# Performance work log

Hardware: AMD Instinct MI355X
Metric: run time of the kernel (lower is better)

Reference implementation:

```python
import jax, jax.numpy as jnp
import numpy as np

FMAP = 32
HEADS = 8
DK = 32
DV = 64
N = FMAP * FMAP  # 1024 tokens
SCALE = DK ** -0.5


def conv1x1(x, W):
    # x: (b,c,h,w), W: (o,c) -> (b,o,h,w)
    return jnp.einsum('bchw,oc->bohw', x, W)


def bn(x, g, b):
    # inference-mode BatchNorm2d folded to per-channel affine
    return x * g[None, :, None, None] + b[None, :, None, None]


def pos_indices():
    r = jnp.arange(FMAP)
    ii, jj = jnp.meshgrid(r, r, indexing='ij')
    pos = jnp.stack([ii.reshape(-1), jj.reshape(-1)], axis=-1)  # (N,2)
    rel = jnp.abs(pos[:, None, :] - pos[None, :, :])            # (N,N,2)
    return rel[..., 0] * FMAP + rel[..., 1]                     # (N,N) int


def setup_inputs() -> dict:
    key = jax.random.key(0)
    ks = jax.random.split(key, 8)
    b, dim = 4, 256
    inner_k, inner_v = HEADS * DK, HEADS * DV
    s = lambda fan: 1.0 / np.sqrt(fan)
    return {
        'x': jax.random.normal(ks[0], (b, dim, FMAP, FMAP), jnp.float32),
        'Wq': jax.random.normal(ks[1], (inner_k, dim), jnp.float32) * s(dim),
        'gq': jnp.ones((inner_k,), jnp.float32), 'bq': jnp.zeros((inner_k,), jnp.float32),
        'Wk': jax.random.normal(ks[2], (inner_k, dim), jnp.float32) * s(dim),
        'gk': jnp.ones((inner_k,), jnp.float32), 'bk': jnp.zeros((inner_k,), jnp.float32),
        'Wv': jax.random.normal(ks[3], (inner_v, dim), jnp.float32) * s(dim),
        'gv': jnp.ones((inner_v,), jnp.float32), 'bv': jnp.zeros((inner_v,), jnp.float32),
        'Wmk': jax.random.normal(ks[4], (HEADS * N, inner_k), jnp.float32) * s(inner_k),
        'gmk': jnp.ones((HEADS * N,), jnp.float32), 'bmk': jnp.zeros((HEADS * N,), jnp.float32),
        'pos_emb': jax.random.normal(ks[5], (N, HEADS), jnp.float32),
        'Wo': jax.random.normal(ks[6], (dim, 2 * inner_v), jnp.float32) * s(2 * inner_v),
        'bo': jnp.zeros((dim,), jnp.float32),
        'go': jnp.ones((dim,), jnp.float32), 'bo2': jnp.zeros((dim,), jnp.float32),
    }


def reference(x, Wq, gq, bq, Wk, gk, bk, Wv, gv, bv, Wmk, gmk, bmk, pos_emb, Wo, bo, go, bo2):
    b = x.shape[0]
    idx = pos_indices()  # (N,N) static

    q1 = bn(conv1x1(x, Wq), gq, bq)                       # (b, h*dk, F, F)
    kk = bn(conv1x1(x, Wk), gk, bk)
    vv = bn(conv1x1(x, Wv), gv, bv)

    # 'b (h d) x y -> b h (x y) d'
    q = q1.reshape(b, HEADS, DK, N).transpose(0, 1, 3, 2)  # (b,h,n,dk)
    k = kk.reshape(b, HEADS, DK, N).transpose(0, 1, 3, 2)
    v = vv.reshape(b, HEADS, DV, N).transpose(0, 1, 3, 2)  # (b,h,n,dv)

    # branch 1: learned conv position logits + relative pos bias
    dots1 = bn(conv1x1(q1, Wmk), gmk, bmk)                 # (b, h*N, F, F)
    dots1 = dots1.reshape(b, HEADS, N, N).transpose(0, 1, 3, 2)  # (b,h,i,j)
    bias = pos_emb[idx]                                    # (N,N,h) gather
    dots1 = dots1 + jnp.transpose(bias, (2, 0, 1))[None] / SCALE
    attn1 = jax.nn.softmax(dots1, axis=-1)

    # branch 2: standard scaled dot-product attention
    dots2 = jnp.einsum('bhid,bhjd->bhij', q, k) * SCALE
    attn2 = jax.nn.softmax(dots2, axis=-1)

    out1 = jnp.einsum('bhij,bhjd->bhid', attn1, v)         # (b,h,n,dv)
    out2 = jnp.einsum('bhij,bhjd->bhid', attn2, v)
    # 'b h (x y) d -> b (h d) x y'
    out1 = out1.transpose(0, 1, 3, 2).reshape(b, HEADS * DV, FMAP, FMAP)
    out2 = out2.transpose(0, 1, 3, 2).reshape(b, HEADS * DV, FMAP, FMAP)

    out = jnp.concatenate([out1, out2], axis=1)            # (b, 2*h*dv, F, F)
    out = jax.nn.gelu(out, approximate=False)
    out = conv1x1(out, Wo) + bo[None, :, None, None]
    return bn(out, go, bo2)
```

## Files before the change

kernel.cpp:

```cpp
#include <hip/hip_runtime.h>

#define NHEADS 8
#define DKK    32
#define DVV    64
#define NTOK   1024
#define DIM    256

typedef float  f32x4 __attribute__((ext_vector_type(4)));
typedef short  s16x4 __attribute__((ext_vector_type(4)));
typedef short  s16x8 __attribute__((ext_vector_type(8)));

__device__ __forceinline__ unsigned short f2bf(float f) {
    unsigned u = __builtin_bit_cast(unsigned, f);
    u += 0x7FFFu + ((u >> 16) & 1u);
    return (unsigned short)(u >> 16);
}

__global__ __launch_bounds__(256) void conv_x(
    const float* __restrict__ x, short* __restrict__ xbt)
{
    __shared__ short tl[64 * 72];
    const int n0 = blockIdx.x * 64, c0 = blockIdx.y * 64, b = blockIdx.z;
    const int tid = threadIdx.x;
    #pragma unroll
    for (int s = 0; s < 16; ++s) {
        int id = tid + s * 256;
        int cc = id >> 6, nn = id & 63;
        tl[nn * 72 + cc] = (short)f2bf(x[(size_t)b * 262144 + (size_t)(c0 + cc) * 1024 + n0 + nn]);
    }
    __syncthreads();
    #pragma unroll
    for (int s = 0; s < 2; ++s) {
        int id = tid + s * 256;
        int nn = id >> 3, c8 = id & 7;
        *(s16x8*)(xbt + ((size_t)b * 1024 + n0 + nn) * 256 + c0 + c8 * 8) =
            *(const s16x8*)&tl[nn * 72 + c8 * 8];
    }
}

__global__ __launch_bounds__(256) void conv_wqkv(
    const float* __restrict__ Wq, const float* __restrict__ gq,
    const float* __restrict__ Wk, const float* __restrict__ gk,
    const float* __restrict__ Wv, const float* __restrict__ gv,
    short* __restrict__ wqkvb)
{
    const int sub = threadIdx.x >> 5;
    const int row = blockIdx.x * 8 + sub;
    const int c0  = (threadIdx.x & 31) * 8;
    float g; const float* src;
    if (row < 256)      { g = gq[row];       src = Wq + (size_t)row * DIM; }
    else if (row < 512) { g = gk[row - 256]; src = Wk + (size_t)(row - 256) * DIM; }
    else                { g = gv[row - 512]; src = Wv + (size_t)(row - 512) * DIM; }
    float4 x0 = *(const float4*)(src + c0);
    float4 x1 = *(const float4*)(src + c0 + 4);
    s16x8 o;
    o[0] = (short)f2bf(g * x0.x); o[1] = (short)f2bf(g * x0.y);
    o[2] = (short)f2bf(g * x0.z); o[3] = (short)f2bf(g * x0.w);
    o[4] = (short)f2bf(g * x1.x); o[5] = (short)f2bf(g * x1.y);
    o[6] = (short)f2bf(g * x1.z); o[7] = (short)f2bf(g * x1.w);
    *(s16x8*)(wqkvb + (size_t)row * DIM + c0) = o;
}

__global__ __launch_bounds__(256) void wmk_convert(
    const float* __restrict__ Wmk, const float* __restrict__ gmk,
    short* __restrict__ out)
{
    const int sub = threadIdx.x >> 5;
    const int ch  = blockIdx.x * 8 + sub;
    const int c0  = (threadIdx.x & 31) * 8;
    const float g = gmk[ch];
    const float* src = Wmk + (size_t)ch * DIM + c0;
    float4 x0 = *(const float4*)(src);
    float4 x1 = *(const float4*)(src + 4);
    s16x8 o;
    o[0] = (short)f2bf(g * x0.x); o[1] = (short)f2bf(g * x0.y);
    o[2] = (short)f2bf(g * x0.z); o[3] = (short)f2bf(g * x0.w);
    o[4] = (short)f2bf(g * x1.x); o[5] = (short)f2bf(g * x1.y);
    o[6] = (short)f2bf(g * x1.z); o[7] = (short)f2bf(g * x1.w);
    *(s16x8*)(out + (size_t)ch * DIM + c0) = o;
}

__global__ __launch_bounds__(256) void conv_wo(
    const float* __restrict__ Wo, short* __restrict__ wob)
{
    const int sub = threadIdx.x >> 5;
    const int row = blockIdx.x * 8 + sub;
    const int l   = threadIdx.x & 31;
    #pragma unroll
    for (int u = 0; u < 4; ++u) {
        int c = l * 8 + u * 256;
        const float* src = Wo + (size_t)row * 1024 + c;
        float4 x0 = *(const float4*)(src);
        float4 x1 = *(const float4*)(src + 4);
        s16x8 o;
        o[0] = (short)f2bf(x0.x); o[1] = (short)f2bf(x0.y);
        o[2] = (short)f2bf(x0.z); o[3] = (short)f2bf(x0.w);
        o[4] = (short)f2bf(x1.x); o[5] = (short)f2bf(x1.y);
        o[6] = (short)f2bf(x1.z); o[7] = (short)f2bf(x1.w);
        *(s16x8*)(wob + (size_t)row * 1024 + c) = o;
    }
}

__global__ __launch_bounds__(256) void qkv_mfma(
    const short* __restrict__ wqkvb, const short* __restrict__ xbt,
    const float* __restrict__ bq, const float* __restrict__ bk,
    const float* __restrict__ bv,
    short* __restrict__ qk_t, short* __restrict__ vvb)
{
    __shared__ __align__(16) short tlds[64 * 136];

    const int t0 = blockIdx.x * 64;
    const int c0 = blockIdx.y * 128;
    const int tid  = threadIdx.x;
    const int w    = tid >> 6, lane = tid & 63;
    const int l15  = lane & 15, lhi = lane >> 4;
    const int wr = w >> 1, wc = w & 1;
    const int cob = c0 + wr * 64;
    const int tob = t0 + wc * 32;

    f32x4 acc[4][2];
    #pragma unroll
    for (int mf = 0; mf < 4; ++mf)
        #pragma unroll
        for (int nf = 0; nf < 2; ++nf) acc[mf][nf] = (f32x4){0.f, 0.f, 0.f, 0.f};

    #pragma unroll
    for (int ks = 0; ks < 8; ++ks) {
        s16x8 af[4], bf[2];
        #pragma unroll
        for (int mf = 0; mf < 4; ++mf)
            af[mf] = *(const s16x8*)(wqkvb + (size_t)(cob + mf * 16 + l15) * DIM + ks * 32 + lhi * 8);
        #pragma unroll
        for (int nf = 0; nf < 2; ++nf)
            bf[nf] = *(const s16x8*)(xbt + (size_t)(tob + nf * 16 + l15) * DIM + ks * 32 + lhi * 8);
        #pragma unroll
        for (int mf = 0; mf < 4; ++mf)
            #pragma unroll
            for (int nf = 0; nf < 2; ++nf)
                acc[mf][nf] = __builtin_amdgcn_mfma_f32_16x16x32_bf16(af[mf], bf[nf], acc[mf][nf], 0, 0, 0);
    }

    float bias[4][4];
    #pragma unroll
    for (int mf = 0; mf < 4; ++mf)
        #pragma unroll
        for (int q = 0; q < 4; ++q) {
            int ch = cob + mf * 16 + lhi * 4 + q;
            bias[mf][q] = (ch < 256) ? bq[ch] : (ch < 512) ? bk[ch - 256] : bv[ch - 512];
        }

    if (c0 < 512) {
        #pragma unroll
        for (int mf = 0; mf < 4; ++mf)
            #pragma unroll
            for (int nf = 0; nf < 2; ++nf) {
                s16x4 pk;
                #pragma unroll
                for (int q = 0; q < 4; ++q)
                    pk[q] = (short)f2bf(acc[mf][nf][q] + bias[mf][q]);
                int tokl = wc * 32 + nf * 16 + l15;
                int chl  = wr * 64 + mf * 16 + lhi * 4;
                *(s16x4*)&tlds[tokl * 136 + chl] = pk;
            }
        __syncthreads();
        #pragma unroll
        for (int s = 0; s < 4; ++s) {
            int id = tid + s * 256;
            int tok = id >> 4, c8 = id & 15;
            *(s16x8*)(qk_t + (size_t)(t0 + tok) * 512 + c0 + c8 * 8) =
                *(const s16x8*)&tlds[tok * 136 + c8 * 8];
        }
    } else {
        #pragma unroll
        for (int mf = 0; mf < 4; ++mf)
            #pragma unroll
            for (int nf = 0; nf < 2; ++nf) {
                int gt = tob + nf * 16 + l15;
                #pragma unroll
                for (int q = 0; q < 4; ++q) {
                    int vch = cob + mf * 16 + lhi * 4 + q - 512;
                    vvb[(size_t)vch * 4096 + gt] = (short)f2bf(acc[mf][nf][q] + bias[mf][q]);
                }
            }
    }
}

__global__ __launch_bounds__(512, 2) void attn_kernel(
    const short* __restrict__ qk_t, const short* __restrict__ vvb,
    const short* __restrict__ wmkb, const float* __restrict__ bmk,
    const float* __restrict__ pos_emb, short* __restrict__ gbuf)
{
    __shared__ __align__(16) short wmks[64 * 264];
    __shared__ __align__(16) short ps[8 * 16 * 72];
    __shared__ float pe_s[1024];
    __shared__ float bmk_s[1024];

    const int it = blockIdx.x, h = blockIdx.y, b = blockIdx.z;
    const int i0  = it * 128;
    const int tid = threadIdx.x;
    const int w    = tid >> 6;
    const int lane = tid & 63;
    const int l15  = lane & 15;
    const int lhi  = lane >> 4;

    for (int p = tid; p < 1024; p += 512) {
        pe_s[p]  = pos_emb[p * NHEADS + h] * 5.656854249492380f;
        bmk_s[p] = bmk[h * NTOK + p];
    }

    const short* q1row = qk_t + ((size_t)b * NTOK + i0 + w * 16 + l15) * 512;
    s16x8 a1[8];
    #pragma unroll
    for (int ks = 0; ks < 8; ++ks)
        a1[ks] = *(const s16x8*)(q1row + ks * 32 + lhi * 8);
    s16x8 a2 = *(const s16x8*)(q1row + h * DKK + lhi * 8);

    int ixq[4], iyq[4];
    #pragma unroll
    for (int q = 0; q < 4; ++q) {
        int i = i0 + w * 16 + lhi * 4 + q;
        ixq[q] = i >> 5; iyq[q] = i & 31;
    }

    f32x4 o1[4], o2[4];
    #pragma unroll
    for (int df = 0; df < 4; ++df)
        #pragma unroll
        for (int q = 0; q < 4; ++q) { o1[df][q] = 0.0f; o2[df][q] = 0.0f; }
    float m1[4], l1[4], m2[4], l2[4];
    #pragma unroll
    for (int q = 0; q < 4; ++q) { m1[q] = -INFINITY; l1[q] = 0.f; m2[q] = -INFINITY; l2[q] = 0.f; }

    const short* kbase = qk_t + (size_t)b * NTOK * 512 + 256 + h * DKK;
    const short* vbase = vvb + (size_t)(h * DVV) * 4096 + b * NTOK;
    const short* wbase = wmkb + (size_t)h * NTOK * DIM;
    short* psw = ps + w * 16 * 72;
    const float SCALE = 0.17677669529663687f;

    __syncthreads();

    for (int jc = 0; jc < 16; ++jc) {
        const int j0 = jc * 64;
        __syncthreads();

        #pragma unroll
        for (int s = 0; s < 4; ++s) {
            int m = tid + s * 512;
            int row = m >> 5, ch = m & 31;
            s16x8 v = *(const s16x8*)(wbase + (size_t)(j0 + row) * DIM + ch * 8);
            *(s16x8*)(&wmks[row * 264 + ch * 8]) = v;
        }
        __syncthreads();

        s16x8 b2f[4], vf[2][4];
        #pragma unroll
        for (int df = 0; df < 4; ++df) {
            b2f[df] = *(const s16x8*)(kbase + (size_t)(j0 + df * 16 + l15) * 512 + lhi * 8);
            #pragma unroll
            for (int ks = 0; ks < 2; ++ks)
                vf[ks][df] = *(const s16x8*)(vbase + (size_t)(df * 16 + l15) * 4096 + j0 + ks * 32 + lhi * 8);
        }

        f32x4 s1[4];
        #pragma unroll
        for (int df = 0; df < 4; ++df) {
            f32x4 acc = {0.f, 0.f, 0.f, 0.f};
            #pragma unroll
            for (int ks = 0; ks < 8; ++ks) {
                s16x8 bfr = *(const s16x8*)(&wmks[(df * 16 + l15) * 264 + ks * 32 + lhi * 8]);
                acc = __builtin_amdgcn_mfma_f32_16x16x32_bf16(a1[ks], bfr, acc, 0, 0, 0);
            }
            s1[df] = acc;
        }
        #pragma unroll
        for (int df = 0; df < 4; ++df) {
            int j  = j0 + df * 16 + l15;
            float bv = bmk_s[j];
            int jx = j >> 5, jy = j & 31;
            #pragma unroll
            for (int q = 0; q < 4; ++q) {
                int dx = ixq[q] - jx; dx = dx < 0 ? -dx : dx;
                int dy = iyq[q] - jy; dy = dy < 0 ? -dy : dy;
                s1[df][q] += bv + pe_s[dx * 32 + dy];
            }
        }
        #pragma unroll
        for (int q = 0; q < 4; ++q) {
            float mx = fmaxf(fmaxf(s1[0][q], s1[1][q]), fmaxf(s1[2][q], s1[3][q]));
            #pragma unroll
            for (int off = 1; off < 16; off <<= 1) mx = fmaxf(mx, __shfl_xor(mx, off, 64));
            float mnew = fmaxf(m1[q], mx);
            float sc = __expf(m1[q] - mnew);
            float rs = 0.f;
            #pragma unroll
            for (int df = 0; df < 4; ++df) {
                float p = __expf(s1[df][q] - mnew);
                rs += p;
                psw[(lhi * 4 + q) * 72 + df * 16 + l15] = (short)f2bf(p);
                o1[df][q] *= sc;
            }
            #pragma unroll
            for (int off = 1; off < 16; off <<= 1) rs += __shfl_xor(rs, off, 64);
            l1[q] = l1[q] * sc + rs;
            m1[q] = mnew;
        }
        {
            s16x8 ap0 = *(const s16x8*)(&psw[l15 * 72 +  0 + lhi * 8]);
            s16x8 ap1 = *(const s16x8*)(&psw[l15 * 72 + 32 + lhi * 8]);
            #pragma unroll
            for (int df = 0; df < 4; ++df) {
                o1[df] = __builtin_amdgcn_mfma_f32_16x16x32_bf16(ap0, vf[0][df], o1[df], 0, 0, 0);
                o1[df] = __builtin_amdgcn_mfma_f32_16x16x32_bf16(ap1, vf[1][df], o1[df], 0, 0, 0);
            }
        }

        f32x4 s2[4];
        #pragma unroll
        for (int df = 0; df < 4; ++df) {
            f32x4 z = {0.f, 0.f, 0.f, 0.f};
            z = __builtin_amdgcn_mfma_f32_16x16x32_bf16(a2, b2f[df], z, 0, 0, 0);
            #pragma unroll
            for (int q = 0; q < 4; ++q) s2[df][q] = z[q] * SCALE;
        }
        #pragma unroll
        for (int q = 0; q < 4; ++q) {
            float mx = fmaxf(fmaxf(s2[0][q], s2[1][q]), fmaxf(s2[2][q], s2[3][q]));
            #pragma unroll
            for (int off = 1; off < 16; off <<= 1) mx = fmaxf(mx, __shfl_xor(mx, off, 64));
            float mnew = fmaxf(m2[q], mx);
            float sc = __expf(m2[q] - mnew);
            float rs = 0.f;
            #pragma unroll
            for (int df = 0; df < 4; ++df) {
                float p = __expf(s2[df][q] - mnew);
                rs += p;
                psw[(lhi * 4 + q) * 72 + df * 16 + l15] = (short)f2bf(p);
                o2[df][q] *= sc;
            }
            #pragma unroll
            for (int off = 1; off < 16; off <<= 1) rs += __shfl_xor(rs, off, 64);
            l2[q] = l2[q] * sc + rs;
            m2[q] = mnew;
        }
        {
            s16x8 ap0 = *(const s16x8*)(&psw[l15 * 72 +  0 + lhi * 8]);
            s16x8 ap1 = *(const s16x8*)(&psw[l15 * 72 + 32 + lhi * 8]);
            #pragma unroll
            for (int df = 0; df < 4; ++df) {
                o2[df] = __builtin_amdgcn_mfma_f32_16x16x32_bf16(ap0, vf[0][df], o2[df], 0, 0, 0);
                o2[df] = __builtin_amdgcn_mfma_f32_16x16x32_bf16(ap1, vf[1][df], o2[df], 0, 0, 0);
            }
        }
    }

    short* osw = wmks;
    #pragma unroll
    for (int pass = 0; pass < 2; ++pass) {
        __syncthreads();
        const int chbase = pass == 0 ? h * DVV : 512 + h * DVV;
        #pragma unroll
        for (int df = 0; df < 4; ++df)
            #pragma unroll
            for (int q = 0; q < 4; ++q) {
                float v = (pass == 0 ? o1[df][q] / l1[q] : o2[df][q] / l2[q]);
                v = 0.5f * v * (1.0f + erff(v * 0.70710678118654752f));
                osw[(w * 16 + lhi * 4 + q) * 72 + df * 16 + l15] = (short)f2bf(v);
            }
        __syncthreads();
        #pragma unroll
        for (int s = 0; s < 2; ++s) {
            int id = tid + s * 512;
            int tok = id >> 3, c8 = id & 7;
            *(s16x8*)(gbuf + ((size_t)b * NTOK + i0 + tok) * 1024 + chbase + c8 * 8) =
                *(const s16x8*)&osw[tok * 72 + c8 * 8];
        }
    }
}

__global__ __launch_bounds__(256) void out_mfma(
    const short* __restrict__ wob, const short* __restrict__ gbuf,
    const float* __restrict__ bo, const float* __restrict__ go,
    const float* __restrict__ bo2, float* __restrict__ out)
{
    const int t0 = blockIdx.x * 64;
    const int c0 = blockIdx.y * 64;
    const int tid  = threadIdx.x;
    const int w    = tid >> 6, lane = tid & 63;
    const int l15  = lane & 15, lhi = lane >> 4;
    const int wr = w >> 1, wc = w & 1;
    const int cob = c0 + wr * 32;
    const int tob = t0 + wc * 32;

    f32x4 acc[2][2];
    #pragma unroll
    for (int mf = 0; mf < 2; ++mf)
        #pragma unroll
        for (int nf = 0; nf < 2; ++nf) acc[mf][nf] = (f32x4){0.f, 0.f, 0.f, 0.f};

    #pragma unroll 4
    for (int ks = 0; ks < 32; ++ks) {
        s16x8 af[2], bf[2];
        #pragma unroll
        for (int mf = 0; mf < 2; ++mf)
            af[mf] = *(const s16x8*)(wob + (size_t)(cob + mf * 16 + l15) * 1024 + ks * 32 + lhi * 8);
        #pragma unroll
        for (int nf = 0; nf < 2; ++nf)
            bf[nf] = *(const s16x8*)(gbuf + (size_t)(tob + nf * 16 + l15) * 1024 + ks * 32 + lhi * 8);
        #pragma unroll
        for (int mf = 0; mf < 2; ++mf)
            #pragma unroll
            for (int nf = 0; nf < 2; ++nf)
                acc[mf][nf] = __builtin_amdgcn_mfma_f32_16x16x32_bf16(af[mf], bf[nf], acc[mf][nf], 0, 0, 0);
    }

    #pragma unroll
    for (int mf = 0; mf < 2; ++mf) {
        #pragma unroll
        for (int q = 0; q < 4; ++q) {
            int co = cob + mf * 16 + lhi * 4 + q;
            float bov = bo[co], gov = go[co], bo2v = bo2[co];
            #pragma unroll
            for (int nf = 0; nf < 2; ++nf) {
                int gt = tob + nf * 16 + l15;
                int bb = gt >> 10, n = gt & 1023;
                out[(size_t)bb * 262144 + (size_t)co * 1024 + n] =
                    fmaf(acc[mf][nf][q] + bov, gov, bo2v);
            }
        }
    }
}

extern "C" void kernel_launch(void* const* d_in, const int* in_sizes, int n_in,
                              void* d_out, int out_size, void* d_ws, size_t ws_size,
                              hipStream_t stream)
{
    const float* x    = (const float*)d_in[0];
    const float* Wq   = (const float*)d_in[1];
    const float* gq   = (const float*)d_in[2];
    const float* bq   = (const float*)d_in[3];
    const float* Wk   = (const float*)d_in[4];
    const float* gk   = (const float*)d_in[5];
    const float* bk   = (const float*)d_in[6];
    const float* Wv   = (const float*)d_in[7];
    const float* gv   = (const float*)d_in[8];
    const float* bv   = (const float*)d_in[9];
    const float* Wmk  = (const float*)d_in[10];
    const float* gmk  = (const float*)d_in[11];
    const float* bmk  = (const float*)d_in[12];
    const float* pe   = (const float*)d_in[13];
    const float* Wo   = (const float*)d_in[14];
    const float* bo   = (const float*)d_in[15];
    const float* go   = (const float*)d_in[16];
    const float* bo2  = (const float*)d_in[17];
    float* out = (float*)d_out;

    char* base = (char*)d_ws;
    short* xbt   = (short*)(base);
    short* wqkvb = (short*)(base + (2u  << 20));
    short* wmkb  = (short*)(base + (3u  << 20));
    short* wob   = (short*)(base + (7u  << 20));
    short* qk_t  = (short*)(base + (8u  << 20));
    short* vvb   = (short*)(base + (12u << 20));
    short* gbuf  = (short*)(base + (16u << 20));

    conv_x<<<dim3(16, 4, 4), 256, 0, stream>>>(x, xbt);
    conv_wqkv<<<dim3(128), 256, 0, stream>>>(Wq, gq, Wk, gk, Wv, gv, wqkvb);
    wmk_convert<<<dim3(1024), 256, 0, stream>>>(Wmk, gmk, wmkb);
    conv_wo<<<dim3(32), 256, 0, stream>>>(Wo, wob);
    qkv_mfma<<<dim3(64, 8), 256, 0, stream>>>(wqkvb, xbt, bq, bk, bv, qk_t, vvb);
    attn_kernel<<<dim3(8, NHEADS, 4), 512, 0, stream>>>(qk_t, vvb, wmkb, bmk, pe, gbuf);
    out_mfma<<<dim3(64, 4), 256, 0, stream>>>(wob, gbuf, bo, go, bo2, out);
}
```

Baseline: 143.1 us.

## Restructure attention with transposed MFMA, register softmax, lazy rescale, and smaller tiles

Rewrites the attention kernel so scores are computed transposed (keys as rows), which keeps the softmax reduction mostly in registers and moves probabilities into the PV MFMA by cross-lane shuffles instead of an LDS round trip. It also prefetches the next Wmk tile into registers during compute, skips the running-max rescale unless the max grows by more than 8, folds the QK scale into the K weights, and uses packed bf16 conversion. The QKV, attention and output GEMMs get smaller tiles and more blocks so more blocks are in flight. Risks include extra register pressure, shuffle overhead, and the lazy-rescale precision tradeoff.

```diff
diff --git a/kernel.cpp b/kernel.cpp
--- a/kernel.cpp
+++ b/kernel.cpp
@@ -9,11 +9,24 @@
 typedef float  f32x4 __attribute__((ext_vector_type(4)));
 typedef short  s16x4 __attribute__((ext_vector_type(4)));
 typedef short  s16x8 __attribute__((ext_vector_type(8)));
+typedef int    i32x4 __attribute__((ext_vector_type(4)));
+
+#define SCALE_QK 0.17677669529663687f
 
 __device__ __forceinline__ unsigned short f2bf(float f) {
     unsigned u = __builtin_bit_cast(unsigned, f);
     u += 0x7FFFu + ((u >> 16) & 1u);
     return (unsigned short)(u >> 16);
+}
+
+__device__ __forceinline__ unsigned cvt_pk_bf16(float lo, float hi) {
+    unsigned r;
+    asm("v_cvt_pk_bf16_f32 %0, %1, %2" : "=v"(r) : "v"(lo), "v"(hi));
+    return r;
+}
+
+__device__ __forceinline__ float gelu(float v) {
+    return 0.5f * v * (1.0f + erff(v * 0.70710678118654752f));
 }
 
 __global__ __launch_bounds__(256) void conv_x(
@@ -48,9 +61,9 @@
     const int row = blockIdx.x * 8 + sub;
     const int c0  = (threadIdx.x & 31) * 8;
     float g; const float* src;
-    if (row < 256)      { g = gq[row];       src = Wq + (size_t)row * DIM; }
-    else if (row < 512) { g = gk[row - 256]; src = Wk + (size_t)(row - 256) * DIM; }
-    else                { g = gv[row - 512]; src = Wv + (size_t)(row - 512) * DIM; }
+    if (row < 256)      { g = gq[row];                  src = Wq + (size_t)row * DIM; }
+    else if (row < 512) { g = gk[row - 256] * SCALE_QK; src = Wk + (size_t)(row - 256) * DIM; }
+    else                { g = gv[row - 512];            src = Wv + (size_t)(row - 512) * DIM; }
     float4 x0 = *(const float4*)(src + c0);
     float4 x1 = *(const float4*)(src + c0 + 4);
     s16x8 o;
@@ -107,64 +120,62 @@
     const float* __restrict__ bv,
     short* __restrict__ qk_t, short* __restrict__ vvb)
 {
-    __shared__ __align__(16) short tlds[64 * 136];
-
-    const int t0 = blockIdx.x * 64;
+    __shared__ __align__(16) short tlds[32 * 136];
+
+    const int t0 = blockIdx.x * 32;
     const int c0 = blockIdx.y * 128;
     const int tid  = threadIdx.x;
     const int w    = tid >> 6, lane = tid & 63;
     const int l15  = lane & 15, lhi = lane >> 4;
-    const int wr = w >> 1, wc = w & 1;
-    const int cob = c0 + wr * 64;
-    const int tob = t0 + wc * 32;
-
-    f32x4 acc[4][2];
-    #pragma unroll
-    for (int mf = 0; mf < 4; ++mf)
+    const int cob = c0 + w * 32;
+
+    f32x4 acc[2][2];
+    #pragma unroll
+    for (int mf = 0; mf < 2; ++mf)
         #pragma unroll
         for (int nf = 0; nf < 2; ++nf) acc[mf][nf] = (f32x4){0.f, 0.f, 0.f, 0.f};
 
     #pragma unroll
     for (int ks = 0; ks < 8; ++ks) {
-        s16x8 af[4], bf[2];
-        #pragma unroll
-        for (int mf = 0; mf < 4; ++mf)
+        s16x8 af[2], bf[2];
+        #pragma unroll
+        for (int mf = 0; mf < 2; ++mf)
             af[mf] = *(const s16x8*)(wqkvb + (size_t)(cob + mf * 16 + l15) * DIM + ks * 32 + lhi * 8);
         #pragma unroll
         for (int nf = 0; nf < 2; ++nf)
-            bf[nf] = *(const s16x8*)(xbt + (size_t)(tob + nf * 16 + l15) * DIM + ks * 32 + lhi * 8);
-        #pragma unroll
-        for (int mf = 0; mf < 4; ++mf)
+            bf[nf] = *(const s16x8*)(xbt + (size_t)(t0 + nf * 16 + l15) * DIM + ks * 32 + lhi * 8);
+        #pragma unroll
+        for (int mf = 0; mf < 2; ++mf)
             #pragma unroll
             for (int nf = 0; nf < 2; ++nf)
                 acc[mf][nf] = __builtin_amdgcn_mfma_f32_16x16x32_bf16(af[mf], bf[nf], acc[mf][nf], 0, 0, 0);
     }
 
-    float bias[4][4];
-    #pragma unroll
-    for (int mf = 0; mf < 4; ++mf)
+    float bias[2][4];
+    #pragma unroll
+    for (int mf = 0; mf < 2; ++mf)
         #pragma unroll
         for (int q = 0; q < 4; ++q) {
             int ch = cob + mf * 16 + lhi * 4 + q;
-            bias[mf][q] = (ch < 256) ? bq[ch] : (ch < 512) ? bk[ch - 256] : bv[ch - 512];
+            bias[mf][q] = (ch < 256) ? bq[ch]
+                        : (ch < 512) ? bk[ch - 256] * SCALE_QK
+                                     : bv[ch - 512];
         }
 
     if (c0 < 512) {
         #pragma unroll
-        for (int mf = 0; mf < 4; ++mf)
+        for (int mf = 0; mf < 2; ++mf)
             #pragma unroll
             for (int nf = 0; nf < 2; ++nf) {
                 s16x4 pk;
                 #pragma unroll
                 for (int q = 0; q < 4; ++q)
                     pk[q] = (short)f2bf(acc[mf][nf][q] + bias[mf][q]);
-                int tokl = wc * 32 + nf * 16 + l15;
-                int chl  = wr * 64 + mf * 16 + lhi * 4;
-                *(s16x4*)&tlds[tokl * 136 + chl] = pk;
+                *(s16x4*)&tlds[(nf * 16 + l15) * 136 + w * 32 + mf * 16 + lhi * 4] = pk;
             }
         __syncthreads();
         #pragma unroll
-        for (int s = 0; s < 4; ++s) {
+        for (int s = 0; s < 2; ++s) {
             int id = tid + s * 256;
             int tok = id >> 4, c8 = id & 15;
             *(s16x8*)(qk_t + (size_t)(t0 + tok) * 512 + c0 + c8 * 8) =
@@ -172,10 +183,10 @@
         }
     } else {
         #pragma unroll
-        for (int mf = 0; mf < 4; ++mf)
+        for (int mf = 0; mf < 2; ++mf)
             #pragma unroll
             for (int nf = 0; nf < 2; ++nf) {
-                int gt = tob + nf * 16 + l15;
+                int gt = t0 + nf * 16 + l15;
                 #pragma unroll
                 for (int q = 0; q < 4; ++q) {
                     int vch = cob + mf * 16 + lhi * 4 + q - 512;
@@ -185,171 +196,206 @@
     }
 }
 
-__global__ __launch_bounds__(512, 2) void attn_kernel(
+__global__ __launch_bounds__(256, 2) void attn_kernel(
     const short* __restrict__ qk_t, const short* __restrict__ vvb,
     const short* __restrict__ wmkb, const float* __restrict__ bmk,
     const float* __restrict__ pos_emb, short* __restrict__ gbuf)
 {
     __shared__ __align__(16) short wmks[64 * 264];
-    __shared__ __align__(16) short ps[8 * 16 * 72];
     __shared__ float pe_s[1024];
     __shared__ float bmk_s[1024];
 
-    const int it = blockIdx.x, h = blockIdx.y, b = blockIdx.z;
-    const int i0  = it * 128;
+    const int flat = blockIdx.x;
+    const int h  = flat & 7;
+    const int it = (flat >> 3) & 15;
+    const int b  = flat >> 7;
+    const int i0 = it * 64;
     const int tid = threadIdx.x;
-    const int w    = tid >> 6;
-    const int lane = tid & 63;
-    const int l15  = lane & 15;
-    const int lhi  = lane >> 4;
-
-    for (int p = tid; p < 1024; p += 512) {
+    const int w = tid >> 6, lane = tid & 63;
+    const int l15 = lane & 15, lhi = lane >> 4;
+
+    for (int p = tid; p < 1024; p += 256) {
         pe_s[p]  = pos_emb[p * NHEADS + h] * 5.656854249492380f;
         bmk_s[p] = bmk[h * NTOK + p];
     }
 
-    const short* q1row = qk_t + ((size_t)b * NTOK + i0 + w * 16 + l15) * 512;
+    const int irow = i0 + w * 16 + l15;
+    const short* q1row = qk_t + ((size_t)b * NTOK + irow) * 512;
     s16x8 a1[8];
     #pragma unroll
     for (int ks = 0; ks < 8; ++ks)
         a1[ks] = *(const s16x8*)(q1row + ks * 32 + lhi * 8);
     s16x8 a2 = *(const s16x8*)(q1row + h * DKK + lhi * 8);
 
-    int ixq[4], iyq[4];
+    const int ix = irow >> 5, iy = irow & 31;
+    int dyv0[4], dyv1[4];
     #pragma unroll
     for (int q = 0; q < 4; ++q) {
-        int i = i0 + w * 16 + lhi * 4 + q;
-        ixq[q] = i >> 5; iyq[q] = i & 31;
+        int j0y = lhi * 4 + q, j1y = 16 + lhi * 4 + q;
+        dyv0[q] = (iy >= j0y) ? iy - j0y : j0y - iy;
+        dyv1[q] = (iy >= j1y) ? iy - j1y : j1y - iy;
     }
 
     f32x4 o1[4], o2[4];
     #pragma unroll
-    for (int df = 0; df < 4; ++df)
-        #pragma unroll
-        for (int q = 0; q < 4; ++q) { o1[df][q] = 0.0f; o2[df][q] = 0.0f; }
-    float m1[4], l1[4], m2[4], l2[4];
-    #pragma unroll
-    for (int q = 0; q < 4; ++q) { m1[q] = -INFINITY; l1[q] = 0.f; m2[q] = -INFINITY; l2[q] = 0.f; }
+    for (int df = 0; df < 4; ++df) { o1[df] = (f32x4){0.f,0.f,0.f,0.f}; o2[df] = (f32x4){0.f,0.f,0.f,0.f}; }
+    float m1 = -INFINITY, l1 = 0.0f, m2 = -INFINITY, l2 = 0.0f;
 
     const short* kbase = qk_t + (size_t)b * NTOK * 512 + 256 + h * DKK;
     const short* vbase = vvb + (size_t)(h * DVV) * 4096 + b * NTOK;
     const short* wbase = wmkb + (size_t)h * NTOK * DIM;
-    short* psw = ps + w * 16 * 72;
-    const float SCALE = 0.17677669529663687f;
-
-    __syncthreads();
+
+    const int srow = tid >> 2;
+    const int scol = (tid & 3) * 64;
+    s16x8 stg[8];
+    #pragma unroll
+    for (int u = 0; u < 8; ++u)
+        stg[u] = *(const s16x8*)(wbase + (size_t)srow * DIM + scol + u * 8);
 
     for (int jc = 0; jc < 16; ++jc) {
         const int j0 = jc * 64;
         __syncthreads();
-
-        #pragma unroll
-        for (int s = 0; s < 4; ++s) {
-            int m = tid + s * 512;
-            int row = m >> 5, ch = m & 31;
-            s16x8 v = *(const s16x8*)(wbase + (size_t)(j0 + row) * DIM + ch * 8);
-            *(s16x8*)(&wmks[row * 264 + ch * 8]) = v;
-        }
+        #pragma unroll
+        for (int u = 0; u < 8; ++u)
+            *(s16x8*)&wmks[srow * 264 + scol + u * 8] = stg[u];
         __syncthreads();
-
-        s16x8 b2f[4], vf[2][4];
-        #pragma unroll
-        for (int df = 0; df < 4; ++df) {
-            b2f[df] = *(const s16x8*)(kbase + (size_t)(j0 + df * 16 + l15) * 512 + lhi * 8);
-            #pragma unroll
-            for (int ks = 0; ks < 2; ++ks)
-                vf[ks][df] = *(const s16x8*)(vbase + (size_t)(df * 16 + l15) * 4096 + j0 + ks * 32 + lhi * 8);
-        }
-
-        f32x4 s1[4];
+        if (jc < 15) {
+            #pragma unroll
+            for (int u = 0; u < 8; ++u)
+                stg[u] = *(const s16x8*)(wbase + (size_t)(j0 + 64 + srow) * DIM + scol + u * 8);
+        }
+
+        s16x8 b2a[4];
+        #pragma unroll
+        for (int df = 0; df < 4; ++df)
+            b2a[df] = *(const s16x8*)(kbase + (size_t)(j0 + df * 16 + l15) * 512 + lhi * 8);
+
+        f32x4 s1T[4];
         #pragma unroll
         for (int df = 0; df < 4; ++df) {
             f32x4 acc = {0.f, 0.f, 0.f, 0.f};
             #pragma unroll
             for (int ks = 0; ks < 8; ++ks) {
-                s16x8 bfr = *(const s16x8*)(&wmks[(df * 16 + l15) * 264 + ks * 32 + lhi * 8]);
-                acc = __builtin_amdgcn_mfma_f32_16x16x32_bf16(a1[ks], bfr, acc, 0, 0, 0);
-            }
-            s1[df] = acc;
-        }
-        #pragma unroll
-        for (int df = 0; df < 4; ++df) {
-            int j  = j0 + df * 16 + l15;
-            float bv = bmk_s[j];
-            int jx = j >> 5, jy = j & 31;
-            #pragma unroll
-            for (int q = 0; q < 4; ++q) {
-                int dx = ixq[q] - jx; dx = dx < 0 ? -dx : dx;
-                int dy = iyq[q] - jy; dy = dy < 0 ? -dy : dy;
-                s1[df][q] += bv + pe_s[dx * 32 + dy];
-            }
-        }
-        #pragma unroll
-        for (int q = 0; q < 4; ++q) {
-            float mx = fmaxf(fmaxf(s1[0][q], s1[1][q]), fmaxf(s1[2][q], s1[3][q]));
-            #pragma unroll
-            for (int off = 1; off < 16; off <<= 1) mx = fmaxf(mx, __shfl_xor(mx, off, 64));
-            float mnew = fmaxf(m1[q], mx);
-            float sc = __expf(m1[q] - mnew);
-            float rs = 0.f;
-            #pragma unroll
-            for (int df = 0; df < 4; ++df) {
-                float p = __expf(s1[df][q] - mnew);
-                rs += p;
-                psw[(lhi * 4 + q) * 72 + df * 16 + l15] = (short)f2bf(p);
-                o1[df][q] *= sc;
-            }
-            #pragma unroll
-            for (int off = 1; off < 16; off <<= 1) rs += __shfl_xor(rs, off, 64);
-            l1[q] = l1[q] * sc + rs;
-            m1[q] = mnew;
-        }
-        {
-            s16x8 ap0 = *(const s16x8*)(&psw[l15 * 72 +  0 + lhi * 8]);
-            s16x8 ap1 = *(const s16x8*)(&psw[l15 * 72 + 32 + lhi * 8]);
-            #pragma unroll
-            for (int df = 0; df < 4; ++df) {
-                o1[df] = __builtin_amdgcn_mfma_f32_16x16x32_bf16(ap0, vf[0][df], o1[df], 0, 0, 0);
-                o1[df] = __builtin_amdgcn_mfma_f32_16x16x32_bf16(ap1, vf[1][df], o1[df], 0, 0, 0);
-            }
-        }
-
-        f32x4 s2[4];
+                s16x8 afr = *(const s16x8*)&wmks[(df * 16 + l15) * 264 + ks * 32 + lhi * 8];
+                acc = __builtin_amdgcn_mfma_f32_16x16x32_bf16(afr, a1[ks], acc, 0, 0, 0);
+            }
+            s1T[df] = acc;
+        }
+        f32x4 s2T[4];
         #pragma unroll
         for (int df = 0; df < 4; ++df) {
             f32x4 z = {0.f, 0.f, 0.f, 0.f};
-            z = __builtin_amdgcn_mfma_f32_16x16x32_bf16(a2, b2f[df], z, 0, 0, 0);
-            #pragma unroll
-            for (int q = 0; q < 4; ++q) s2[df][q] = z[q] * SCALE;
-        }
-        #pragma unroll
-        for (int q = 0; q < 4; ++q) {
-            float mx = fmaxf(fmaxf(s2[0][q], s2[1][q]), fmaxf(s2[2][q], s2[3][q]));
-            #pragma unroll
-            for (int off = 1; off < 16; off <<= 1) mx = fmaxf(mx, __shfl_xor(mx, off, 64));
-            float mnew = fmaxf(m2[q], mx);
-            float sc = __expf(m2[q] - mnew);
+            s2T[df] = __builtin_amdgcn_mfma_f32_16x16x32_bf16(b2a[df], a2, z, 0, 0, 0);
+        }
+
+        {
+            const int jx0 = j0 >> 5;
+            int d0 = ix - jx0;     d0 = d0 < 0 ? -d0 : d0;
+            int d1 = ix - jx0 - 1; d1 = d1 < 0 ? -d1 : d1;
+            const float* per0 = pe_s + d0 * 32;
+            const float* per1 = pe_s + d1 * 32;
+            #pragma unroll
+            for (int df = 0; df < 4; ++df) {
+                f32x4 bm4 = *(const f32x4*)&bmk_s[j0 + df * 16 + lhi * 4];
+                #pragma unroll
+                for (int q = 0; q < 4; ++q) {
+                    int dy = (df & 1) ? dyv1[q] : dyv0[q];
+                    float pv = (df < 2) ? per0[dy] : per1[dy];
+                    s1T[df][q] += bm4[q] + pv;
+                }
+            }
+        }
+
+        unsigned pk1[4][2];
+        {
+            float mx = s1T[0][0];
+            #pragma unroll
+            for (int df = 0; df < 4; ++df)
+                #pragma unroll
+                for (int q = 0; q < 4; ++q) mx = fmaxf(mx, s1T[df][q]);
+            mx = fmaxf(mx, __shfl_xor(mx, 16));
+            mx = fmaxf(mx, __shfl_xor(mx, 32));
+            float tm = fmaxf(m1, mx);
+            if (!__all(tm - m1 <= 8.0f)) {
+                float sc = __expf(m1 - tm);
+                l1 *= sc;
+                #pragma unroll
+                for (int df = 0; df < 4; ++df) o1[df] *= sc;
+                m1 = tm;
+            }
             float rs = 0.f;
             #pragma unroll
             for (int df = 0; df < 4; ++df) {
-                float p = __expf(s2[df][q] - mnew);
-                rs += p;
-                psw[(lhi * 4 + q) * 72 + df * 16 + l15] = (short)f2bf(p);
-                o2[df][q] *= sc;
-            }
-            #pragma unroll
-            for (int off = 1; off < 16; off <<= 1) rs += __shfl_xor(rs, off, 64);
-            l2[q] = l2[q] * sc + rs;
-            m2[q] = mnew;
-        }
+                float p0 = __expf(s1T[df][0] - m1), p1 = __expf(s1T[df][1] - m1);
+                float p2 = __expf(s1T[df][2] - m1), p3 = __expf(s1T[df][3] - m1);
+                rs += (p0 + p1) + (p2 + p3);
+                pk1[df][0] = cvt_pk_bf16(p0, p1);
+                pk1[df][1] = cvt_pk_bf16(p2, p3);
+            }
+            rs += __shfl_xor(rs, 16);
+            rs += __shfl_xor(rs, 32);
+            l1 += rs;
+        }
+        unsigned pk2[4][2];
         {
-            s16x8 ap0 = *(const s16x8*)(&psw[l15 * 72 +  0 + lhi * 8]);
-            s16x8 ap1 = *(const s16x8*)(&psw[l15 * 72 + 32 + lhi * 8]);
+            float mx = s2T[0][0];
+            #pragma unroll
+            for (int df = 0; df < 4; ++df)
+                #pragma unroll
+                for (int q = 0; q < 4; ++q) mx = fmaxf(mx, s2T[df][q]);
+            mx = fmaxf(mx, __shfl_xor(mx, 16));
+            mx = fmaxf(mx, __shfl_xor(mx, 32));
+            float tm = fmaxf(m2, mx);
+            if (!__all(tm - m2 <= 8.0f)) {
+                float sc = __expf(m2 - tm);
+                l2 *= sc;
+                #pragma unroll
+                for (int df = 0; df < 4; ++df) o2[df] *= sc;
+                m2 = tm;
+            }
+            float rs = 0.f;
             #pragma unroll
             for (int df = 0; df < 4; ++df) {
-                o2[df] = __builtin_amdgcn_mfma_f32_16x16x32_bf16(ap0, vf[0][df], o2[df], 0, 0, 0);
-                o2[df] = __builtin_amdgcn_mfma_f32_16x16x32_bf16(ap1, vf[1][df], o2[df], 0, 0, 0);
-            }
+                float p0 = __expf(s2T[df][0] - m2), p1 = __expf(s2T[df][1] - m2);
+                float p2 = __expf(s2T[df][2] - m2), p3 = __expf(s2T[df][3] - m2);
+                rs += (p0 + p1) + (p2 + p3);
+                pk2[df][0] = cvt_pk_bf16(p0, p1);
+                pk2[df][1] = cvt_pk_bf16(p2, p3);
+            }
+            rs += __shfl_xor(rs, 16);
+            rs += __shfl_xor(rs, 32);
+            l2 += rs;
+        }
+
+        const int srcA = l15 + ((lane & 16) << 1);
+        const bool hi = (lane & 32) != 0;
+        #pragma unroll
+        for (int kt = 0; kt < 2; ++kt) {
+            s16x8 vf[4];
+            #pragma unroll
+            for (int df = 0; df < 4; ++df)
+                vf[df] = *(const s16x8*)(vbase + (size_t)(df * 16 + l15) * 4096 + j0 + kt * 32 + lhi * 8);
+
+            int x0 = __shfl((int)pk1[2*kt][0], srcA),      x1 = __shfl((int)pk1[2*kt+1][0], srcA);
+            int y0 = __shfl((int)pk1[2*kt][1], srcA),      y1 = __shfl((int)pk1[2*kt+1][1], srcA);
+            int z0 = __shfl((int)pk1[2*kt][0], srcA + 16), z1 = __shfl((int)pk1[2*kt+1][0], srcA + 16);
+            int u0 = __shfl((int)pk1[2*kt][1], srcA + 16), u1 = __shfl((int)pk1[2*kt+1][1], srcA + 16);
+            i32x4 bd1 = { hi ? x1 : x0, hi ? y1 : y0, hi ? z1 : z0, hi ? u1 : u0 };
+            s16x8 pb1 = __builtin_bit_cast(s16x8, bd1);
+
+            x0 = __shfl((int)pk2[2*kt][0], srcA);      x1 = __shfl((int)pk2[2*kt+1][0], srcA);
+            y0 = __shfl((int)pk2[2*kt][1], srcA);      y1 = __shfl((int)pk2[2*kt+1][1], srcA);
+            z0 = __shfl((int)pk2[2*kt][0], srcA + 16); z1 = __shfl((int)pk2[2*kt+1][0], srcA + 16);
+            u0 = __shfl((int)pk2[2*kt][1], srcA + 16); u1 = __shfl((int)pk2[2*kt+1][1], srcA + 16);
+            i32x4 bd2 = { hi ? x1 : x0, hi ? y1 : y0, hi ? z1 : z0, hi ? u1 : u0 };
+            s16x8 pb2 = __builtin_bit_cast(s16x8, bd2);
+
+            #pragma unroll
+            for (int df = 0; df < 4; ++df)
+                o1[df] = __builtin_amdgcn_mfma_f32_16x16x32_bf16(vf[df], pb1, o1[df], 0, 0, 0);
+            #pragma unroll
+            for (int df = 0; df < 4; ++df)
+                o2[df] = __builtin_amdgcn_mfma_f32_16x16x32_bf16(vf[df], pb2, o2[df], 0, 0, 0);
         }
     }
 
@@ -357,22 +403,25 @@
     #pragma unroll
     for (int pass = 0; pass < 2; ++pass) {
         __syncthreads();
-        const int chbase = pass == 0 ? h * DVV : 512 + h * DVV;
+        const int chbase = (pass ? 512 : 0) + h * DVV;
+        const float inv = 1.0f / (pass ? l2 : l1);
         #pragma unroll
         for (int df = 0; df < 4; ++df)
             #pragma unroll
-            for (int q = 0; q < 4; ++q) {
-                float v = (pass == 0 ? o1[df][q] / l1[q] : o2[df][q] / l2[q]);
-                v = 0.5f * v * (1.0f + erff(v * 0.70710678118654752f));
-                osw[(w * 16 + lhi * 4 + q) * 72 + df * 16 + l15] = (short)f2bf(v);
+            for (int r = 0; r < 2; ++r) {
+                float v0 = gelu((pass ? o2 : o1)[df][2*r]     * inv);
+                float v1 = gelu((pass ? o2 : o1)[df][2*r + 1] * inv);
+                unsigned d = cvt_pk_bf16(v0, v1);
+                *(unsigned*)&osw[(w * 16 + l15) * 72 + df * 16 + lhi * 4 + 2 * r] = d;
             }
         __syncthreads();
-        #pragma unroll
-        for (int s = 0; s < 2; ++s) {
-            int id = tid + s * 512;
-            int tok = id >> 3, c8 = id & 7;
-            *(s16x8*)(gbuf + ((size_t)b * NTOK + i0 + tok) * 1024 + chbase + c8 * 8) =
-                *(const s16x8*)&osw[tok * 72 + c8 * 8];
+        {
+            int i = tid >> 2, cb = (tid & 3) * 16;
+            s16x8 v0 = *(const s16x8*)&osw[i * 72 + cb];
+            s16x8 v1 = *(const s16x8*)&osw[i * 72 + cb + 8];
+            size_t dst = ((size_t)b * NTOK + i0 + i) * 1024 + chbase + cb;
+            *(s16x8*)(gbuf + dst)     = v0;
+            *(s16x8*)(gbuf + dst + 8) = v1;
         }
     }
 }
@@ -382,52 +431,38 @@
     const float* __restrict__ bo, const float* __restrict__ go,
     const float* __restrict__ bo2, float* __restrict__ out)
 {
-    const int t0 = blockIdx.x * 64;
+    const int t0 = blockIdx.x * 32;
     const int c0 = blockIdx.y * 64;
     const int tid  = threadIdx.x;
     const int w    = tid >> 6, lane = tid & 63;
     const int l15  = lane & 15, lhi = lane >> 4;
     const int wr = w >> 1, wc = w & 1;
     const int cob = c0 + wr * 32;
-    const int tob = t0 + wc * 32;
-
-    f32x4 acc[2][2];
-    #pragma unroll
-    for (int mf = 0; mf < 2; ++mf)
-        #pragma unroll
-        for (int nf = 0; nf < 2; ++nf) acc[mf][nf] = (f32x4){0.f, 0.f, 0.f, 0.f};
+    const int tob = t0 + wc * 16;
+
+    f32x4 acc[2];
+    acc[0] = (f32x4){0.f, 0.f, 0.f, 0.f};
+    acc[1] = (f32x4){0.f, 0.f, 0.f, 0.f};
 
     #pragma unroll 4
     for (int ks = 0; ks < 32; ++ks) {
-        s16x8 af[2], bf[2];
-        #pragma unroll
-        for (int mf = 0; mf < 2; ++mf)
-            af[mf] = *(const s16x8*)(wob + (size_t)(cob + mf * 16 + l15) * 1024 + ks * 32 + lhi * 8);
-        #pragma unroll
-        for (int nf = 0; nf < 2; ++nf)
-            bf[nf] = *(const s16x8*)(gbuf + (size_t)(tob + nf * 16 + l15) * 1024 + ks * 32 + lhi * 8);
-        #pragma unroll
-        for (int mf = 0; mf < 2; ++mf)
-            #pragma unroll
-            for (int nf = 0; nf < 2; ++nf)
-                acc[mf][nf] = __builtin_amdgcn_mfma_f32_16x16x32_bf16(af[mf], bf[nf], acc[mf][nf], 0, 0, 0);
-    }
-
-    #pragma unroll
-    for (int mf = 0; mf < 2; ++mf) {
+        s16x8 af0 = *(const s16x8*)(wob + (size_t)(cob + l15) * 1024 + ks * 32 + lhi * 8);
+        s16x8 af1 = *(const s16x8*)(wob + (size_t)(cob + 16 + l15) * 1024 + ks * 32 + lhi * 8);
+        s16x8 bf  = *(const s16x8*)(gbuf + (size_t)(tob + l15) * 1024 + ks * 32 + lhi * 8);
+        acc[0] = __builtin_amdgcn_mfma_f32_16x16x32_bf16(af0, bf, acc[0], 0, 0, 0);
+        acc[1] = __builtin_amdgcn_mfma_f32_16x16x32_bf16(af1, bf, acc[1], 0, 0, 0);
+    }
+
+    const int gt = tob + l15;
+    const int bb = gt >> 10, n = gt & 1023;
+    #pragma unroll
+    for (int mf = 0; mf < 2; ++mf)
         #pragma unroll
         for (int q = 0; q < 4; ++q) {
             int co = cob + mf * 16 + lhi * 4 + q;
-            float bov = bo[co], gov = go[co], bo2v = bo2[co];
-            #pragma unroll
-            for (int nf = 0; nf < 2; ++nf) {
-                int gt = tob + nf * 16 + l15;
-                int bb = gt >> 10, n = gt & 1023;
-                out[(size_t)bb * 262144 + (size_t)co * 1024 + n] =
-                    fmaf(acc[mf][nf][q] + bov, gov, bo2v);
-            }
-        }
-    }
+            out[(size_t)bb * 262144 + (size_t)co * 1024 + n] =
+                fmaf(acc[mf][q] + bo[co], go[co], bo2[co]);
+        }
 }
 
 extern "C" void kernel_launch(void* const* d_in, const int* in_sizes, int n_in,
@@ -467,7 +502,7 @@
     conv_wqkv<<<dim3(128), 256, 0, stream>>>(Wq, gq, Wk, gk, Wv, gv, wqkvb);
     wmk_convert<<<dim3(1024), 256, 0, stream>>>(Wmk, gmk, wmkb);
     conv_wo<<<dim3(32), 256, 0, stream>>>(Wo, wob);
-    qkv_mfma<<<dim3(64, 8), 256, 0, stream>>>(wqkvb, xbt, bq, bk, bv, qk_t, vvb);
-    attn_kernel<<<dim3(8, NHEADS, 4), 512, 0, stream>>>(qk_t, vvb, wmkb, bmk, pe, gbuf);
-    out_mfma<<<dim3(64, 4), 256, 0, stream>>>(wob, gbuf, bo, go, bo2, out);
-}
+    qkv_mfma<<<dim3(128, 8), 256, 0, stream>>>(wqkvb, xbt, bq, bk, bv, qk_t, vvb);
+    attn_kernel<<<dim3(512), 256, 0, stream>>>(qk_t, vvb, wmkb, bmk, pe, gbuf);
+    out_mfma<<<dim3(128, 4), 256, 0, stream>>>(wob, gbuf, bo, go, bo2, out);
+}
```

New measurement: 153.3 us. 7.1% more time.
